# Kernel optimization log

Hardware: AMD Instinct MI355X
Metric: run time of the kernel (lower is better)

The kernel has to match this reference:

```python
import jax, jax.numpy as jnp
import numpy as np

DIM = 2048
ATT_DIM = 2048
N_HEADS = 16
HEAD_DIM = ATT_DIM // N_HEADS  # 128


def setup_inputs() -> dict:
    key = jax.random.key(0)
    k1, k2, k3 = jax.random.split(key, 3)
    tgt_len = 2048
    x = jax.random.normal(k1, (tgt_len, DIM), dtype=jnp.float32)
    # nn.Linear weights: [out_features, in_features], no bias
    w_in = jax.random.normal(k2, (3 * ATT_DIM, DIM), dtype=jnp.float32) * (1.0 / np.sqrt(DIM))
    w_out = jax.random.normal(k3, (DIM, ATT_DIM), dtype=jnp.float32) * (1.0 / np.sqrt(ATT_DIM))
    return {"x": x, "w_in": w_in, "w_out": w_out, "tgt_len": tgt_len}


def reference(x, w_in, w_out, tgt_len):
    # qkv projection: Linear -> x @ W^T, then split into thirds
    qkv = x @ w_in.T                      # [T, 3*att_dim]
    q, k, v = jnp.split(qkv, 3, axis=-1)  # each [T, att_dim]
    # [T, H, Dh] -> [H, T, Dh]
    q = q.reshape(tgt_len, N_HEADS, HEAD_DIM).transpose(1, 0, 2)
    k = k.reshape(tgt_len, N_HEADS, HEAD_DIM).transpose(1, 0, 2)
    v = v.reshape(tgt_len, N_HEADS, HEAD_DIM).transpose(1, 0, 2)
    scaling = 1.0 / jnp.sqrt(jnp.asarray(HEAD_DIM, dtype=x.dtype))
    scores = jnp.einsum("htd,hsd->hts", q, k) * scaling  # [H, T, T]
    attn = jax.nn.softmax(scores, axis=-1)
    ctx = jnp.einsum("hts,hsd->htd", attn, v)             # [H, T, Dh]
    ctx = ctx.transpose(1, 0, 2).reshape(tgt_len, ATT_DIM)
    return ctx @ w_out.T                                   # [T, dim]
```

## Files before the change

### kernel.cpp

```cpp
#include <hip/hip_runtime.h>

#define T_LEN 2048
#define DIM 2048
#define NH 16
#define HD 128
#define QKV_LD 6144

typedef __attribute__((ext_vector_type(8))) short short8;
typedef __attribute__((ext_vector_type(4))) short short4v;
typedef __attribute__((ext_vector_type(4))) float f32x4;
typedef __attribute__((ext_vector_type(4))) float float4v;
typedef __attribute__((ext_vector_type(4))) unsigned short ushort4v;
typedef __attribute__((ext_vector_type(2))) unsigned int uint2v;

static __device__ __forceinline__ unsigned short f2bf(float f) {
  unsigned u = __builtin_bit_cast(unsigned, f);
  u += 0x7fffu + ((u >> 16) & 1u);
  return (unsigned short)(u >> 16);
}

static __device__ __forceinline__ float max3f(float a, float b, float c) {
  return fmaxf(fmaxf(a, b), c);
}

static __device__ __forceinline__ f32x4 mfma16(short8 a, short8 b, f32x4 c) {
  return __builtin_amdgcn_mfma_f32_16x16x32_bf16(a, b, c, 0, 0, 0);
}

#define GLDS16(SRC, DST)                                                            \
  __builtin_amdgcn_global_load_lds((__attribute__((address_space(1))) void*)(SRC),  \
                                   (__attribute__((address_space(3))) void*)(DST),  \
                                   16, 0, 0)

__global__ void cast3_f32_bf16(const float* __restrict__ a, unsigned short* __restrict__ oa, int na4,
                               const float* __restrict__ b, unsigned short* __restrict__ ob, int nb4,
                               const float* __restrict__ c, unsigned short* __restrict__ oc, int nc4) {
  const int stride = gridDim.x * blockDim.x;
  const int g = blockIdx.x * blockDim.x + threadIdx.x;
#define CAST_LOOP(SRC, DST, N4)                                  \
  for (int i = g; i < (N4); i += stride) {                       \
    float4v f = ((const float4v*)(SRC))[i];                      \
    ushort4v o;                                                  \
    o.x = f2bf(f.x); o.y = f2bf(f.y);                            \
    o.z = f2bf(f.z); o.w = f2bf(f.w);                            \
    ((ushort4v*)(DST))[i] = o;                                   \
  }
  CAST_LOOP(a, oa, na4)
  CAST_LOOP(b, ob, nb4)
  CAST_LOOP(c, oc, nc4)
#undef CAST_LOOP
}

template <int MODE>
__global__ __launch_bounds__(256) void gemm_bt_128(
    const unsigned short* __restrict__ A,
    const unsigned short* __restrict__ B,
    void* __restrict__ Cv, unsigned short* __restrict__ vt,
    int M, int N, int K) {
  __shared__ unsigned short As[128 * 64];
  __shared__ unsigned short Bs[128 * 64];
  const int tid = threadIdx.x;
  const int wave = tid >> 6;
  const int lane = tid & 63;
  const int l15 = lane & 15, l16 = lane >> 4;
  const int bm = blockIdx.y * 128;
  const int bn = blockIdx.x * 128;
  const int wr = wave >> 1, wc = wave & 1;

  f32x4 acc[4][4] = {};

  int srow[4], scol[4];
#pragma unroll
  for (int i = 0; i < 4; ++i) {
    int lin = i * 4096 + tid * 16;
    int row = lin >> 7;
    int cb = lin & 127;
    srow[i] = row;
    scol[i] = (cb ^ ((row & 7) << 4)) >> 1;
  }

  for (int k0 = 0; k0 < K; k0 += 64) {
#pragma unroll
    for (int i = 0; i < 4; ++i) {
      GLDS16(A + (size_t)(bm + srow[i]) * K + k0 + scol[i], As + i * 2048 + wave * 512);
      GLDS16(B + (size_t)(bn + srow[i]) * K + k0 + scol[i], Bs + i * 2048 + wave * 512);
    }
    __syncthreads();
#pragma unroll
    for (int kk = 0; kk < 2; ++kk) {
      const int cb = kk * 64 + l16 * 16;
      short8 af[4], bfr[4];
#pragma unroll
      for (int m = 0; m < 4; ++m) {
        int row = wr * 64 + m * 16 + l15;
        af[m] = *(const short8*)((const char*)As + row * 128 + (cb ^ ((row & 7) << 4)));
      }
#pragma unroll
      for (int n = 0; n < 4; ++n) {
        int row = wc * 64 + n * 16 + l15;
        bfr[n] = *(const short8*)((const char*)Bs + row * 128 + (cb ^ ((row & 7) << 4)));
      }
#pragma unroll
      for (int m = 0; m < 4; ++m)
#pragma unroll
        for (int n = 0; n < 4; ++n)
          acc[m][n] = mfma16(af[m], bfr[n], acc[m][n]);
    }
    __syncthreads();
  }

  const bool vthird = (MODE == 2) && (bn >= 2 * DIM);
#pragma unroll
  for (int m = 0; m < 4; ++m)
#pragma unroll
    for (int n = 0; n < 4; ++n) {
      int row = bm + wr * 64 + m * 16 + l16 * 4;
      int col = bn + wc * 64 + n * 16 + l15;
      if (MODE == 2 && vthird) {
        short4v w;
#pragma unroll
        for (int j = 0; j < 4; ++j) w[j] = (short)f2bf(acc[m][n][j]);
        *(short4v*)(vt + (size_t)(col - 2 * DIM) * T_LEN + row) = w;
      } else {
#pragma unroll
        for (int j = 0; j < 4; ++j) {
          if (MODE == 0)
            ((float*)Cv)[(size_t)(row + j) * N + col] = acc[m][n][j];
          else
            ((unsigned short*)Cv)[(size_t)(row + j) * N + col] = f2bf(acc[m][n][j]);
        }
      }
    }
}

__global__ __launch_bounds__(256) void attn_fwd(
    const unsigned short* __restrict__ qkv,
    const unsigned short* __restrict__ vt,
    unsigned short* __restrict__ ctx) {
  __shared__ unsigned short Ks[2][64 * 128];
  __shared__ unsigned short Vs[2][128 * 64];
  __shared__ unsigned short Ps[4 * 16 * 64];
  const int tid = threadIdx.x;
  const int wave = tid >> 6;
  const int lane = tid & 63;
  const int l15 = lane & 15, l16 = lane >> 4;

  const int wg = blockIdx.y * 32 + blockIdx.x;
  const int swz = (wg & 7) * 64 + (wg >> 3);
  const int h = swz >> 5;
  const int q0 = (swz & 31) * 64 + wave * 16;
  const float SCL = 0.08838834764831845f * 1.4426950408889634f;

  short8 qf[4];
#pragma unroll
  for (int kk = 0; kk < 4; ++kk)
    qf[kk] = *(const short8*)(qkv + (size_t)(q0 + l15) * QKV_LD + h * HD + kk * 32 + l16 * 8);

  f32x4 acc_o[8] = {};
  float m_r = -1e30f;
  float l_r = 0.f;

  int krow[4], kcol[4], vrow[4], vcol[4];
#pragma unroll
  for (int i = 0; i < 4; ++i) {
    int lin = i * 4096 + tid * 16;
    int r = lin >> 8;
    int cb = lin & 255;
    krow[i] = r; kcol[i] = (cb ^ ((r & 7) << 4)) >> 1;
    r = lin >> 7;
    cb = lin & 127;
    vrow[i] = r; vcol[i] = (cb ^ ((r & 7) << 4)) >> 1;
  }
  const unsigned short* kbase = qkv + 2048 + h * HD;
  const unsigned short* vbase = vt + (size_t)h * HD * T_LEN;

#define STAGE_KV(BUF, S0)                                                              \
  do {                                                                                 \
    _Pragma("unroll")                                                                  \
    for (int i = 0; i < 4; ++i) {                                                      \
      GLDS16(kbase + (size_t)((S0) + krow[i]) * QKV_LD + kcol[i],                      \
             Ks[BUF] + i * 2048 + wave * 512);                                         \
      GLDS16(vbase + (size_t)vrow[i] * T_LEN + (S0) + vcol[i],                         \
             Vs[BUF] + i * 2048 + wave * 512);                                         \
    }                                                                                  \
  } while (0)

  STAGE_KV(0, 0);
  __syncthreads();

  const int NT = T_LEN / 64;
  int cur = 0;
  for (int t = 0; t < NT; ++t) {
    if (t + 1 < NT) STAGE_KV(cur ^ 1, (t + 1) * 64);

    const unsigned short* ks = Ks[cur];
    const unsigned short* vs = Vs[cur];

    f32x4 st[4] = {};
#pragma unroll
    for (int c = 0; c < 4; ++c) {
#pragma unroll
      for (int kk = 0; kk < 4; ++kk) {
        int row = c * 16 + l15;
        int cb = kk * 64 + l16 * 16;
        short8 kf = *(const short8*)((const char*)ks + row * 256 + (cb ^ ((row & 7) << 4)));
        st[c] = mfma16(kf, qf[kk], st[c]);
      }
    }

    float ma = max3f(st[0][0], st[0][1], st[0][2]);
    float mb = max3f(st[0][3], st[1][0], st[1][1]);
    float mc = max3f(st[1][2], st[1][3], st[2][0]);
    float md = max3f(st[2][1], st[2][2], st[2][3]);
    float me = max3f(st[3][0], st[3][1], st[3][2]);
    float pmax = fmaxf(max3f(ma, mb, mc), max3f(md, me, st[3][3])) * SCL;
    pmax = fmaxf(pmax, __shfl_xor(pmax, 16));
    pmax = fmaxf(pmax, __shfl_xor(pmax, 32));

    if (!__all(pmax - m_r <= 8.0f)) {
      float nm = fmaxf(m_r, pmax);
      float corr = __builtin_amdgcn_exp2f(m_r - nm);
      m_r = nm;
      l_r *= corr;
      float cj[4];
#pragma unroll
      for (int j = 0; j < 4; ++j) cj[j] = __shfl(corr, l16 * 4 + j);
#pragma unroll
      for (int d = 0; d < 8; ++d)
#pragma unroll
        for (int j = 0; j < 4; ++j) acc_o[d][j] *= cj[j];
    }

    float p[4][4];
#pragma unroll
    for (int c = 0; c < 4; ++c)
#pragma unroll
      for (int j = 0; j < 4; ++j)
        p[c][j] = __builtin_amdgcn_exp2f(st[c][j] * SCL - m_r);
    float s01 = (p[0][0] + p[0][1]) + (p[0][2] + p[0][3]);
    float s23 = (p[1][0] + p[1][1]) + (p[1][2] + p[1][3]);
    float s45 = (p[2][0] + p[2][1]) + (p[2][2] + p[2][3]);
    float s67 = (p[3][0] + p[3][1]) + (p[3][2] + p[3][3]);
    float tsum = (s01 + s23) + (s45 + s67);
    tsum += __shfl_xor(tsum, 16);
    tsum += __shfl_xor(tsum, 32);
    l_r += tsum;

    char* pbase = (char*)Ps + wave * 2048;
#pragma unroll
    for (int c = 0; c < 4; ++c) {
      uint2v w;
      w.x = (unsigned)f2bf(p[c][0]) | ((unsigned)f2bf(p[c][1]) << 16);
      w.y = (unsigned)f2bf(p[c][2]) | ((unsigned)f2bf(p[c][3]) << 16);
      int off = l15 * 128 + c * 32 + l16 * 8;
      *(uint2v*)(pbase + (off ^ ((l15 & 7) << 4))) = w;
    }

#pragma unroll
    for (int kk = 0; kk < 2; ++kk) {
      int cb = kk * 64 + l16 * 16;
      short8 pa = *(const short8*)(pbase + l15 * 128 + (cb ^ ((l15 & 7) << 4)));
#pragma unroll
      for (int d = 0; d < 8; ++d) {
        int row = d * 16 + l15;
        short8 vb = *(const short8*)((const char*)vs + row * 128 + (cb ^ ((row & 7) << 4)));
        acc_o[d] = mfma16(pa, vb, acc_o[d]);
      }
    }

    __syncthreads();
    cur ^= 1;
  }
#undef STAGE_KV

  float lq[4];
#pragma unroll
  for (int j = 0; j < 4; ++j) lq[j] = 1.0f / __shfl(l_r, l16 * 4 + j);
#pragma unroll
  for (int d = 0; d < 8; ++d)
#pragma unroll
    for (int j = 0; j < 4; ++j) {
      int row = q0 + l16 * 4 + j;
      int col = h * HD + d * 16 + l15;
      ctx[(size_t)row * DIM + col] = f2bf(acc_o[d][j] * lq[j]);
    }
}

extern "C" void kernel_launch(void* const* d_in, const int* in_sizes, int n_in,
                              void* d_out, int out_size, void* d_ws, size_t ws_size,
                              hipStream_t stream) {
  const float* x = (const float*)d_in[0];
  const float* w_in = (const float*)d_in[1];
  const float* w_out = (const float*)d_in[2];

  char* ws = (char*)d_ws;
  unsigned short* xbf  = (unsigned short*)(ws + 0);
  unsigned short* wibf = (unsigned short*)(ws + 8388608);
  unsigned short* wobf = (unsigned short*)(ws + 33554432);
  unsigned short* qkv  = (unsigned short*)(ws + 41943040);
  unsigned short* ctx  = (unsigned short*)(ws + 67108864);
  unsigned short* vt   = (unsigned short*)(ws + 75497472);

  cast3_f32_bf16<<<2048, 256, 0, stream>>>(
      x, xbf, (T_LEN * DIM) / 4,
      w_in, wibf, (3 * DIM * DIM) / 4,
      w_out, wobf, (DIM * DIM) / 4);

  gemm_bt_128<2><<<dim3(48, 16), 256, 0, stream>>>(
      xbf, wibf, (void*)qkv, vt, T_LEN, 3 * DIM, DIM);
  attn_fwd<<<dim3(32, 16), 256, 0, stream>>>(qkv, vt, ctx);
  gemm_bt_128<0><<<dim3(16, 16), 256, 0, stream>>>(
      ctx, wobf, d_out, nullptr, T_LEN, DIM, DIM);
}
```

Measured before the change: 183.0 us.

## Split attention over key halves and merge partials in a combine kernel

Attention now runs in two halves along the key axis, doubling the workgroup count from 512 to 1024. Each half writes unnormalized bf16 partial outputs plus row max and sum, and a new combine kernel merges them and normalizes. V is no longer staged through LDS; each lane reads it directly from global memory inside the PV loop, which frees LDS but adds uncoalesced global latency. The change also adds an extra launch and extra partial-output traffic, and rounds the partials to bf16 before they are combined.

```diff
diff --git a/kernel.cpp b/kernel.cpp
--- a/kernel.cpp
+++ b/kernel.cpp
@@ -17,6 +17,11 @@
   unsigned u = __builtin_bit_cast(unsigned, f);
   u += 0x7fffu + ((u >> 16) & 1u);
   return (unsigned short)(u >> 16);
+}
+
+static __device__ __forceinline__ float bf2f(unsigned short u) {
+  unsigned x = ((unsigned)u) << 16;
+  return __builtin_bit_cast(float, x);
 }
 
 static __device__ __forceinline__ float max3f(float a, float b, float c) {
@@ -136,19 +141,21 @@
 __global__ __launch_bounds__(256) void attn_fwd(
     const unsigned short* __restrict__ qkv,
     const unsigned short* __restrict__ vt,
-    unsigned short* __restrict__ ctx) {
+    unsigned short* __restrict__ po,
+    float* __restrict__ ml) {
   __shared__ unsigned short Ks[2][64 * 128];
-  __shared__ unsigned short Vs[2][128 * 64];
   __shared__ unsigned short Ps[4 * 16 * 64];
   const int tid = threadIdx.x;
   const int wave = tid >> 6;
   const int lane = tid & 63;
   const int l15 = lane & 15, l16 = lane >> 4;
 
-  const int wg = blockIdx.y * 32 + blockIdx.x;
-  const int swz = (wg & 7) * 64 + (wg >> 3);
-  const int h = swz >> 5;
+  const int wg = blockIdx.y * 64 + blockIdx.x;
+  const int swz = (wg & 7) * 128 + (wg >> 3);
+  const int h = swz >> 6;
+  const int half = (swz >> 5) & 1;
   const int q0 = (swz & 31) * 64 + wave * 16;
+  const int s_begin = half * (T_LEN / 2);
   const float SCL = 0.08838834764831845f * 1.4426950408889634f;
 
   short8 qf[4];
@@ -160,41 +167,35 @@
   float m_r = -1e30f;
   float l_r = 0.f;
 
-  int krow[4], kcol[4], vrow[4], vcol[4];
+  const unsigned short* kp[4];
 #pragma unroll
   for (int i = 0; i < 4; ++i) {
     int lin = i * 4096 + tid * 16;
     int r = lin >> 8;
     int cb = lin & 255;
-    krow[i] = r; kcol[i] = (cb ^ ((r & 7) << 4)) >> 1;
-    r = lin >> 7;
-    cb = lin & 127;
-    vrow[i] = r; vcol[i] = (cb ^ ((r & 7) << 4)) >> 1;
-  }
-  const unsigned short* kbase = qkv + 2048 + h * HD;
-  const unsigned short* vbase = vt + (size_t)h * HD * T_LEN;
-
-#define STAGE_KV(BUF, S0)                                                              \
+    kp[i] = qkv + 2048 + h * HD + (size_t)(s_begin + r) * QKV_LD + ((cb ^ ((r & 7) << 4)) >> 1);
+  }
+  const unsigned short* vrp = vt + (size_t)h * HD * T_LEN + (size_t)l15 * T_LEN +
+                              s_begin + l16 * 8;
+
+#define STAGE_K(BUF)                                                                   \
   do {                                                                                 \
     _Pragma("unroll")                                                                  \
     for (int i = 0; i < 4; ++i) {                                                      \
-      GLDS16(kbase + (size_t)((S0) + krow[i]) * QKV_LD + kcol[i],                      \
-             Ks[BUF] + i * 2048 + wave * 512);                                         \
-      GLDS16(vbase + (size_t)vrow[i] * T_LEN + (S0) + vcol[i],                         \
-             Vs[BUF] + i * 2048 + wave * 512);                                         \
+      GLDS16(kp[i], Ks[BUF] + i * 2048 + wave * 512);                                  \
+      kp[i] += 64 * QKV_LD;                                                            \
     }                                                                                  \
   } while (0)
 
-  STAGE_KV(0, 0);
+  STAGE_K(0);
   __syncthreads();
 
-  const int NT = T_LEN / 64;
+  const int NT = (T_LEN / 2) / 64;
   int cur = 0;
   for (int t = 0; t < NT; ++t) {
-    if (t + 1 < NT) STAGE_KV(cur ^ 1, (t + 1) * 64);
+    if (t + 1 < NT) STAGE_K(cur ^ 1);
 
     const unsigned short* ks = Ks[cur];
-    const unsigned short* vs = Vs[cur];
 
     f32x4 st[4] = {};
 #pragma unroll
@@ -256,14 +257,14 @@
       *(uint2v*)(pbase + (off ^ ((l15 & 7) << 4))) = w;
     }
 
+    const unsigned short* vtile = vrp + t * 64;
 #pragma unroll
     for (int kk = 0; kk < 2; ++kk) {
       int cb = kk * 64 + l16 * 16;
       short8 pa = *(const short8*)(pbase + l15 * 128 + (cb ^ ((l15 & 7) << 4)));
 #pragma unroll
       for (int d = 0; d < 8; ++d) {
-        int row = d * 16 + l15;
-        short8 vb = *(const short8*)((const char*)vs + row * 128 + (cb ^ ((row & 7) << 4)));
+        short8 vb = *(const short8*)(vtile + (size_t)d * 16 * T_LEN + kk * 32);
         acc_o[d] = mfma16(pa, vb, acc_o[d]);
       }
     }
@@ -271,19 +272,44 @@
     __syncthreads();
     cur ^= 1;
   }
-#undef STAGE_KV
-
-  float lq[4];
-#pragma unroll
-  for (int j = 0; j < 4; ++j) lq[j] = 1.0f / __shfl(l_r, l16 * 4 + j);
+#undef STAGE_K
+
+  const size_t pb = ((size_t)half * NH * T_LEN + (size_t)h * T_LEN) * HD;
 #pragma unroll
   for (int d = 0; d < 8; ++d)
 #pragma unroll
     for (int j = 0; j < 4; ++j) {
-      int row = q0 + l16 * 4 + j;
-      int col = h * HD + d * 16 + l15;
-      ctx[(size_t)row * DIM + col] = f2bf(acc_o[d][j] * lq[j]);
-    }
+      int q = q0 + l16 * 4 + j;
+      po[pb + (size_t)q * HD + d * 16 + l15] = f2bf(acc_o[d][j]);
+    }
+  if (l16 == 0) {
+    size_t mlbase = ((size_t)half * NH * T_LEN + (size_t)h * T_LEN + q0 + l15) * 2;
+    ml[mlbase] = m_r;
+    ml[mlbase + 1] = l_r;
+  }
+}
+
+__global__ __launch_bounds__(256) void attn_combine(
+    const unsigned short* __restrict__ po, const float* __restrict__ ml,
+    unsigned short* __restrict__ ctx) {
+  const int g = blockIdx.x * 256 + threadIdx.x;
+  const int hq = g >> 4;
+  const int oct = g & 15;
+  const float m0 = ml[hq * 2], l0 = ml[hq * 2 + 1];
+  const float m1 = ml[NH * T_LEN * 2 + hq * 2], l1 = ml[NH * T_LEN * 2 + hq * 2 + 1];
+  const float m = fmaxf(m0, m1);
+  float a0 = __builtin_amdgcn_exp2f(m0 - m);
+  float a1 = __builtin_amdgcn_exp2f(m1 - m);
+  const float rl = 1.0f / (l0 * a0 + l1 * a1);
+  a0 *= rl; a1 *= rl;
+  const short8 o0 = *(const short8*)(po + (size_t)hq * HD + oct * 8);
+  const short8 o1 = *(const short8*)(po + (size_t)NH * T_LEN * HD + (size_t)hq * HD + oct * 8);
+  short8 w;
+#pragma unroll
+  for (int j = 0; j < 8; ++j)
+    w[j] = (short)f2bf(bf2f((unsigned short)o0[j]) * a0 + bf2f((unsigned short)o1[j]) * a1);
+  const int h = hq >> 11, q = hq & (T_LEN - 1);
+  *(short8*)(ctx + (size_t)q * DIM + h * HD + oct * 8) = w;
 }
 
 extern "C" void kernel_launch(void* const* d_in, const int* in_sizes, int n_in,
@@ -300,6 +326,8 @@
   unsigned short* qkv  = (unsigned short*)(ws + 41943040);
   unsigned short* ctx  = (unsigned short*)(ws + 67108864);
   unsigned short* vt   = (unsigned short*)(ws + 75497472);
+  unsigned short* po   = (unsigned short*)(ws + 0);
+  float*          ml   = (float*)(ws + 16777216);
 
   cast3_f32_bf16<<<2048, 256, 0, stream>>>(
       x, xbf, (T_LEN * DIM) / 4,
@@ -308,7 +336,8 @@
 
   gemm_bt_128<2><<<dim3(48, 16), 256, 0, stream>>>(
       xbf, wibf, (void*)qkv, vt, T_LEN, 3 * DIM, DIM);
-  attn_fwd<<<dim3(32, 16), 256, 0, stream>>>(qkv, vt, ctx);
+  attn_fwd<<<dim3(64, 16), 256, 0, stream>>>(qkv, vt, po, ml);
+  attn_combine<<<2048, 256, 0, stream>>>(po, ml, ctx);
   gemm_bt_128<0><<<dim3(16, 16), 256, 0, stream>>>(
       ctx, wobf, d_out, nullptr, T_LEN, DIM, DIM);
 }
```

Result: slower. 255.8 us (+39.8%).
